# Performance work log

Hardware: AMD Instinct MI355X
Metric: run time of the kernel (lower is better)

Reference implementation:

```python
import jax, jax.numpy as jnp
import numpy as np

N, E, IN, H0, H1 = 50000, 1600000, 64, 64, 128


def _gcn(h, W, b, row, col):
    # PyG GCNConv, add_self_loops=False, unit edge weights:
    # out[col] += d^{-1/2}[row] * d^{-1/2}[col] * (h @ W)[row]; bias added after aggregation
    n = h.shape[0]
    deg = jnp.zeros((n,), h.dtype).at[col].add(jnp.ones((row.shape[0],), h.dtype))
    dinv = jnp.where(deg > 0, jax.lax.rsqrt(jnp.maximum(deg, 1e-12)), 0.0)
    norm = (dinv[row] * dinv[col])[:, None]  # [E,1]
    m = h @ W  # transform before propagate (small GEMM)
    out = jnp.zeros((n, W.shape[1]), h.dtype).at[col].add(norm * m[row])
    return out + b


def _bn(h, g, b):
    # BatchNorm1d training-mode math (biased variance), eps=1e-5
    mu = h.mean(0)
    var = ((h - mu) ** 2).mean(0)
    return g * (h - mu) * jax.lax.rsqrt(var + 1e-5) + b


def _san(h):
    return jnp.nan_to_num(h, nan=0.0, posinf=100.0, neginf=-100.0)


def _slice(x, ei, W0, b0, W1, b1, res1, g0, be0, g1, be1):
    row, col = ei[0], ei[1]
    # layer 0: conv -> bn -> relu -> (dropout=eval identity) -> residual (Identity, 64==64) -> nan_to_num
    h1 = _san(jax.nn.relu(_bn(_gcn(x, W0, b0, row, col), g0, be0)) + x)
    # layer 1 (last): conv -> bn -> residual (Linear proj 64->128, no bias) -> nan_to_num
    h2 = _san(_bn(_gcn(h1, W1, b1, row, col), g1, be1) + h1 @ res1)
    return h2


def setup_inputs() -> dict:
    k = jax.random.split(jax.random.key(0), 16)
    f = lambda kk, sh, s: jax.random.normal(kk, sh, jnp.float32) * s
    return {
        "x": f(k[0], (N, IN), 1.0),
        "edge_index0": jax.random.randint(k[1], (2, E), 0, N),
        "edge_index1": jax.random.randint(k[2], (2, E), 0, N),
        "w0_s0": f(k[3], (IN, H0), 0.1), "b0_s0": jnp.zeros((H0,), jnp.float32),
        "w1_s0": f(k[4], (H0, H1), 0.1), "b1_s0": jnp.zeros((H1,), jnp.float32),
        "res1_s0": f(k[5], (H0, H1), 0.1),
        "w0_s1": f(k[6], (IN, H0), 0.1), "b0_s1": jnp.zeros((H0,), jnp.float32),
        "w1_s1": f(k[7], (H0, H1), 0.1), "b1_s1": jnp.zeros((H1,), jnp.float32),
        "res1_s1": f(k[8], (H0, H1), 0.1),
        "bn_g0": jnp.ones((H0,), jnp.float32), "bn_b0": jnp.zeros((H0,), jnp.float32),
        "bn_g1": jnp.ones((H1,), jnp.float32), "bn_b1": jnp.zeros((H1,), jnp.float32),
        "fc1_w": f(k[9], (2 * H1, H1), 0.1), "fc1_b": jnp.zeros((H1,), jnp.float32),
        "fc2_w": f(k[10], (H1, 2), 0.1), "fc2_b": jnp.zeros((2,), jnp.float32),
    }


def reference(x, edge_index0, edge_index1,
              w0_s0, b0_s0, w1_s0, b1_s0, res1_s0,
              w0_s1, b0_s1, w1_s1, b1_s1, res1_s1,
              bn_g0, bn_b0, bn_g1, bn_b1,
              fc1_w, fc1_b, fc2_w, fc2_b):
    out0 = _slice(x, edge_index0, w0_s0, b0_s0, w1_s0, b1_s0, res1_s0, bn_g0, bn_b0, bn_g1, bn_b1)
    out1 = _slice(x, edge_index1, w0_s1, b0_s1, w1_s1, b1_s1, res1_s1, bn_g0, bn_b0, bn_g1, bn_b1)
    combined = jnp.concatenate([out0, out1], axis=1)  # [N, 2*H1]
    h = jax.nn.relu(combined @ fc1_w + fc1_b)  # dropout is eval-mode identity
    logits = h @ fc2_w + fc2_b
    return logits, jax.nn.softmax(logits, axis=1)
```

## Files before the change

kernel.cpp:

```cpp
#include <hip/hip_runtime.h>
#include <hip/hip_bf16.h>
#include <math.h>


typedef short v8s __attribute__((ext_vector_type(8)));
typedef float f32x4 __attribute__((ext_vector_type(4)));

#define BSTRIDE 10240

__device__ __forceinline__ float sanf(float v) {
    if (v != v) return 0.f;
    if (isinf(v)) return v > 0.f ? 100.f : -100.f;
    return v;
}

__device__ __forceinline__ unsigned short bf16of(float v) {
    __hip_bfloat16 h = __float2bfloat16(v);
    return *(unsigned short*)&h;
}
__device__ __forceinline__ unsigned pack2(float lo, float hi) {
    return (unsigned)bf16of(lo) | ((unsigned)bf16of(hi) << 16);
}
__device__ __forceinline__ float uflo(unsigned u) { return __uint_as_float(u << 16); }
__device__ __forceinline__ float ufhi(unsigned u) { return __uint_as_float(u & 0xFFFF0000u); }

__device__ __forceinline__ void packone(const float* __restrict__ src, unsigned* __restrict__ dst,
                                        int L, int Khalf, int F) {
    int c = L / Khalf, kp = L - c * Khalf;
    dst[L] = pack2(src[(2 * kp) * F + c], src[(2 * kp + 1) * F + c]);
}

__global__ __launch_bounds__(256) void prep_kernel(const float* __restrict__ w0_0,
                                                   const float* __restrict__ w0_1,
                                                   const float* __restrict__ w1_0,
                                                   const float* __restrict__ w1_1,
                                                   const float* __restrict__ r_0,
                                                   const float* __restrict__ r_1,
                                                   const float* __restrict__ fc1,
                                                   unsigned* __restrict__ wpk,
                                                   int* __restrict__ bcnt,
                                                   float* __restrict__ sums) {
    int gid = blockIdx.x * 256 + threadIdx.x;
    if (gid < 512) bcnt[gid] = 0;
    if (gid < 8192) sums[gid] = 0.f;
    if (gid < 2048)       packone(w0_0, wpk + 0,     gid - 0,     32, 64);
    else if (gid < 4096)  packone(w0_1, wpk + 2048,  gid - 2048,  32, 64);
    else if (gid < 8192)  packone(w1_0, wpk + 4096,  gid - 4096,  32, 128);
    else if (gid < 12288) packone(w1_1, wpk + 8192,  gid - 8192,  32, 128);
    else if (gid < 16384) packone(r_0,  wpk + 12288, gid - 12288, 32, 128);
    else if (gid < 20480) packone(r_1,  wpk + 16384, gid - 16384, 32, 128);
    else if (gid < 36864) packone(fc1,  wpk + 20480, gid - 20480, 128, 128);
}


__global__ __launch_bounds__(512) void kC_bin(const int* __restrict__ ei0,
                                              const int* __restrict__ ei1,
                                              int* __restrict__ bcnt,
                                              unsigned* __restrict__ binned,
                                              int E, int n) {
    __shared__ int cnt[512];
    __shared__ int base[512];
    int t = threadIdx.x;
    cnt[t] = 0;
    int E2 = 2 * E;
    int e0 = blockIdx.x * 8192;
    unsigned pk[16];
    int bk[16];
    __syncthreads();
#pragma unroll
    for (int j = 0; j < 16; ++j) {
        int ge = e0 + t + j * 512;
        bk[j] = -1;
        if (ge < E2) {
            int slice = ge >= E;
            const int* ei = slice ? ei1 : ei0;
            int e = ge - slice * E;
            int col = ei[E + e], row = ei[e];
            int gcol = slice * n + col;
            bk[j] = gcol >> 8;
            pk[j] = (unsigned)row | (((unsigned)gcol & 255u) << 16);
            atomicAdd(&cnt[bk[j]], 1);
        }
    }
    __syncthreads();
    {
        int c = cnt[t];
        base[t] = c ? atomicAdd(&bcnt[t], c) : 0;
    }
    __syncthreads();
    cnt[t] = 0;
    __syncthreads();
#pragma unroll
    for (int j = 0; j < 16; ++j) {
        if (bk[j] >= 0) {
            int loc = atomicAdd(&cnt[bk[j]], 1);
            int off = base[bk[j]] + loc;
            if (off < BSTRIDE) binned[(size_t)bk[j] * BSTRIDE + off] = pk[j];
        }
    }
}

__global__ __launch_bounds__(512) void kD_build(const unsigned* __restrict__ binned,
                                                const int* __restrict__ bcnt,
                                                const float* __restrict__ x,
                                                int* __restrict__ rowptr,
                                                float* __restrict__ dinv,
                                                unsigned short* __restrict__ csr,
                                                unsigned short* __restrict__ xsb,
                                                int n2, int NB) {
    __shared__ int pref[512];
    __shared__ int cnt[256];
    __shared__ int scn[256];
    __shared__ int cur[256];
    __shared__ float ds[256];
    int b = blockIdx.x, t = threadIdx.x;
    int n = n2 >> 1, n64 = n * 64;
    pref[t] = (t < NB) ? bcnt[t] : 0;
    __syncthreads();
    for (int off = 1; off < 512; off <<= 1) {
        int u = (t >= off) ? pref[t - off] : 0;
        __syncthreads();
        pref[t] += u;
        __syncthreads();
    }
    int s = (b > 0) ? pref[b - 1] : 0;
    int e = pref[b];
    int m = e - s;
    const unsigned* seg = binned + (size_t)b * BSTRIDE;
    if (t < 256) cnt[t] = 0;
    __syncthreads();
    for (int i = t; i < m; i += 512) atomicAdd(&cnt[(seg[i] >> 16) & 255], 1);
    __syncthreads();
    int v = (t < 256) ? cnt[t] : 0;
    if (t < 256) scn[t] = v;
    __syncthreads();
    for (int off = 1; off < 256; off <<= 1) {
        int u = (t < 256 && t >= off) ? scn[t - off] : 0;
        __syncthreads();
        if (t < 256) scn[t] += u;
        __syncthreads();
    }
    if (t < 256) {
        int excl = scn[t] - v;
        int gcol = b * 256 + t;
        float dv = v > 0 ? rsqrtf((float)v) : 0.f;
        ds[t] = dv;
        if (gcol < n2) {
            rowptr[gcol] = s + excl;
            dinv[gcol] = dv;
        }
        cur[t] = excl;
    }
    __syncthreads();
    for (int i = t; i < m; i += 512) {
        unsigned p = seg[i];
        int cl = (p >> 16) & 255;
        int pos = s + atomicAdd(&cur[cl], 1);
        csr[pos] = (unsigned short)(p & 0xFFFFu);
    }
    if (b == NB - 1 && t == 0) rowptr[n2] = e;
    for (int k = t; k < 2048; k += 512) {
        int gl = k >> 3, segk = k & 7;
        int gcol = b * 256 + gl;
        if (gcol >= n2) continue;
        float d = ds[gl];
        int slice = gcol >= n;
        int row = gcol - slice * n;
        const float* xp = x + (size_t)row * 64 + segk * 8;
        float4 v0 = *(const float4*)xp;
        float4 v1 = *(const float4*)(xp + 4);
        uint4 o;
        o.x = pack2(v0.x * d, v0.y * d); o.y = pack2(v0.z * d, v0.w * d);
        o.z = pack2(v1.x * d, v1.y * d); o.w = pack2(v1.z * d, v1.w * d);
        *(uint4*)&xsb[(size_t)slice * n64 + (size_t)row * 64 + segk * 8] = o;
    }
}


#define LOAD8(U, IDX)                                                       \
    do {                                                                    \
        _Pragma("unroll") for (int j = 0; j < 8; ++j) {                     \
            int r = __shfl((IDX), j, 8);                                    \
            (U)[j] = *(const uint4*)&mb[(size_t)r * 64 + l * 8];            \
        }                                                                   \
    } while (0)
#define ZPAD8(U, BB)                                                        \
    do {                                                                    \
        _Pragma("unroll") for (int j = 0; j < 8; ++j)                       \
            if ((BB) + j >= e) { (U)[j].x = 0; (U)[j].y = 0;                \
                                 (U)[j].z = 0; (U)[j].w = 0; }              \
    } while (0)
#define ACC8(U)                                                             \
    do {                                                                    \
        _Pragma("unroll") for (int j = 0; j < 8; ++j) {                     \
            a0 += uflo((U)[j].x); a1 += ufhi((U)[j].x);                     \
            a2 += uflo((U)[j].y); a3 += ufhi((U)[j].y);                     \
            a4 += uflo((U)[j].z); a5 += ufhi((U)[j].z);                     \
            a6 += uflo((U)[j].w); a7 += ufhi((U)[j].w);                     \
        }                                                                   \
    } while (0)

__global__ __launch_bounds__(256) void gatherbf_kernel(const int* __restrict__ rowptr,
                                                       const unsigned short* __restrict__ csr,
                                                       const unsigned short* __restrict__ xsb,
                                                       const float* __restrict__ dinv,
                                                       unsigned short* __restrict__ outb,
                                                       int n) {
    int blk = blockIdx.x;
    int xcd = blk & 7;
    int slice = (xcd >= 4) ? 1 : 0;
    int rank = (blk >> 3) * 4 + (xcd & 3);
    int nodeLocal = rank * 32 + (threadIdx.x >> 3);
    if (nodeLocal >= n) return;
    int node = slice * n + nodeLocal;
    int l = threadIdx.x & 7;
    const unsigned short* mb = xsb + (size_t)slice * n * 64;
    int s = rowptr[node], e = rowptr[node + 1];
    float a0 = 0.f, a1 = 0.f, a2 = 0.f, a3 = 0.f, a4 = 0.f, a5 = 0.f, a6 = 0.f, a7 = 0.f;
    uint4 uA[8], uB[8];
    int b = s;
    if (b + 8 <= e) {
        int ia = csr[b + l];
        LOAD8(uA, ia);
        int bB = b + 8;
        int ib = (bB + l < e) ? (int)csr[bB + l] : 0;
        while (true) {
            bool hasB = (bB < e);
            if (hasB) {
                LOAD8(uB, ib);
                if (bB + 8 > e) ZPAD8(uB, bB);
            }
            int bA2 = bB + 8;
            if (bA2 < e) ia = (bA2 + l < e) ? (int)csr[bA2 + l] : 0;
            ACC8(uA);
            if (!hasB) break;
            bool hasA2 = (bA2 < e);
            if (hasA2) {
                LOAD8(uA, ia);
                if (bA2 + 8 > e) ZPAD8(uA, bA2);
            }
            int bB2 = bA2 + 8;
            if (bB2 < e) ib = (bB2 + l < e) ? (int)csr[bB2 + l] : 0;
            ACC8(uB);
            if (!hasA2) break;
            bB = bB2;
        }
    } else if (b < e) {
        int ia = (b + l < e) ? (int)csr[b + l] : 0;
        LOAD8(uA, ia);
        ZPAD8(uA, b);
        ACC8(uA);
    }
    float d = dinv[node];
    uint4 o;
    o.x = pack2(a0 * d, a1 * d);
    o.y = pack2(a2 * d, a3 * d);
    o.z = pack2(a4 * d, a5 * d);
    o.w = pack2(a6 * d, a7 * d);
    *(uint4*)&outb[(size_t)node * 64 + l * 8] = o;
}


template <int F>
__global__ __launch_bounds__(256) void mfma_gemmb(const unsigned short* __restrict__ Ab,
                                                  const unsigned* __restrict__ WT0,
                                                  const unsigned* __restrict__ WT1,
                                                  unsigned short* __restrict__ Cb,
                                                  float* __restrict__ sums_base,
                                                  int roff, int n) {
    constexpr int NC = F / 16;
    __shared__ float ls[2 * F];
    __shared__ unsigned short stb[64 * F];
    int BPS = (n + 63) >> 6;
    int slice = blockIdx.x >= BPS;
    int sb = blockIdx.x - slice * BPS;
    const unsigned* WT = slice ? WT1 : WT0;
    int row0 = slice * n + sb * 64;
    int rows = min(64, n - sb * 64);
    for (int i = threadIdx.x; i < 2 * F; i += 256) ls[i] = 0.f;
    int w = threadIdx.x >> 6, lane = threadIdx.x & 63, q = lane >> 4, ln = lane & 15;
    const unsigned* A32 = (const unsigned*)Ab;
    size_t arow = (size_t)(row0 + 16 * w + ln) * 32;
    v8s af0 = *(const v8s*)&A32[arow + q * 4];
    v8s af1 = *(const v8s*)&A32[arow + 16 + q * 4];
    f32x4 acc[NC];
#pragma unroll
    for (int ct = 0; ct < NC; ++ct) acc[ct] = {0.f, 0.f, 0.f, 0.f};
#pragma unroll
    for (int ct = 0; ct < NC; ++ct) {
        v8s b0 = *(const v8s*)&WT[(ct * 16 + ln) * 32 + q * 4];
        v8s b1 = *(const v8s*)&WT[(ct * 16 + ln) * 32 + 16 + q * 4];
        acc[ct] = __builtin_amdgcn_mfma_f32_16x16x32_bf16(af0, b0, acc[ct], 0, 0, 0);
        acc[ct] = __builtin_amdgcn_mfma_f32_16x16x32_bf16(af1, b1, acc[ct], 0, 0, 0);
    }
    __syncthreads();
#pragma unroll
    for (int ct = 0; ct < NC; ++ct) {
        float s1 = 0.f, s2 = 0.f;
        int cc = ct * 16 + ln;
#pragma unroll
        for (int i = 0; i < 4; ++i) {
            int r = 16 * w + q * 4 + i;
            stb[r * F + (cc ^ ((r & 7) << 3))] = bf16of(acc[ct][i]);
            if (r < rows) {
                float v = acc[ct][i];
                s1 += v;
                s2 += v * v;
            }
        }
        s1 += __shfl_xor(s1, 16); s1 += __shfl_xor(s1, 32);
        s2 += __shfl_xor(s2, 16); s2 += __shfl_xor(s2, 32);
        if (q == 0) {
            atomicAdd(&ls[cc], s1);
            atomicAdd(&ls[F + cc], s2);
        }
    }
    __syncthreads();
    {
        constexpr int CPT = F / 4;
        int rr = threadIdx.x >> 2, sg = threadIdx.x & 3;
        if (rr < rows) {
            int swz = (rr & 7) << 3;
            int cb = sg * CPT;
            uint4* dst = (uint4*)(Cb + (size_t)(row0 + rr) * F + cb);
#pragma unroll
            for (int jj = 0; jj < CPT / 8; ++jj)
                dst[jj] = *(const uint4*)&stb[rr * F + ((cb + jj * 8) ^ swz)];
        }
    }
    if (threadIdx.x < F) {
        float* dst = sums_base + (blockIdx.x & 7) * 1024 + roff + slice * 2 * F;
        unsafeAtomicAdd(&dst[threadIdx.x], ls[threadIdx.x]);
        unsafeAtomicAdd(&dst[F + threadIdx.x], ls[F + threadIdx.x]);
    }
}

__global__ __launch_bounds__(256) void apply0_kernel(const unsigned short* __restrict__ t0b,
                                                     const float* __restrict__ x,
                                                     const float* __restrict__ sums_base,
                                                     const float* __restrict__ g,
                                                     const float* __restrict__ be,
                                                     const float* __restrict__ dinv,
                                                     unsigned short* __restrict__ h1b,
                                                     unsigned short* __restrict__ h1sb,
                                                     int n64, int total, int n) {
    __shared__ float sc[256];
    int t = threadIdx.x;
    if (t < 128) {
        int slice = t >> 6, f = t & 63;
        float s1 = 0.f, s2 = 0.f;
#pragma unroll
        for (int r = 0; r < 8; ++r) {
            const float* src = sums_base + r * 1024 + 512 + slice * 128;
            s1 += src[f];
            s2 += src[64 + f];
        }
        float inv_n = 1.0f / (float)n;
        float mu = s1 * inv_n;
        float var = fmaxf(s2 * inv_n - mu * mu, 0.f);
        float scale = g[f] * rsqrtf(var + 1e-5f);
        sc[slice * 128 + f] = scale;
        sc[slice * 128 + 64 + f] = be[f] - mu * scale;
    }
    __syncthreads();
    int i8 = (blockIdx.x * 256 + t) * 8;
    if (i8 >= total) return;
    int slice = i8 >= n64;
    int f0 = i8 & 63;
    const float* scp = sc + slice * 128;
    uint4 tv = *(const uint4*)&t0b[i8];
    const float* xp = x + (i8 - slice * n64);
    float4 x0 = *(const float4*)xp;
    float4 x1 = *(const float4*)(xp + 4);
    float4 s0 = *(const float4*)&scp[f0];
    float4 s1 = *(const float4*)&scp[f0 + 4];
    float4 g0 = *(const float4*)&scp[64 + f0];
    float4 g1 = *(const float4*)&scp[64 + f0 + 4];
    float d = dinv[i8 >> 6];
    float tvv[8] = {uflo(tv.x), ufhi(tv.x), uflo(tv.y), ufhi(tv.y),
                    uflo(tv.z), ufhi(tv.z), uflo(tv.w), ufhi(tv.w)};
    float sa[8] = {s0.x, s0.y, s0.z, s0.w, s1.x, s1.y, s1.z, s1.w};
    float sh[8] = {g0.x, g0.y, g0.z, g0.w, g1.x, g1.y, g1.z, g1.w};
    float xv[8] = {x0.x, x0.y, x0.z, x0.w, x1.x, x1.y, x1.z, x1.w};
    unsigned po[4], ps[4];
#pragma unroll
    for (int j = 0; j < 4; ++j) {
        float a = sanf(fmaxf(fmaf(tvv[2 * j], sa[2 * j], sh[2 * j]), 0.f) + xv[2 * j]);
        float b = sanf(fmaxf(fmaf(tvv[2 * j + 1], sa[2 * j + 1], sh[2 * j + 1]), 0.f) + xv[2 * j + 1]);
        po[j] = pack2(a, b);
        ps[j] = pack2(a * d, b * d);
    }
    *(uint4*)&h1b[i8] = *(uint4*)po;
    *(uint4*)&h1sb[i8] = *(uint4*)ps;
}

__global__ __launch_bounds__(256) void apply1_head(const unsigned short* __restrict__ h1b,
                                                   const unsigned short* __restrict__ Tb,
                                                   const unsigned* __restrict__ RT0,
                                                   const unsigned* __restrict__ RT1,
                                                   const unsigned* __restrict__ FT,
                                                   const float* __restrict__ sums_base,
                                                   const float* __restrict__ g,
                                                   const float* __restrict__ be,
                                                   const float* __restrict__ fc1_b,
                                                   const float* __restrict__ w2,
                                                   const float* __restrict__ b2,
                                                   float* __restrict__ out, int n) {
    __shared__ float st[64 * 128];
    __shared__ unsigned short cmb[64 * 256];
    __shared__ float scl[512];
    int t = threadIdx.x;
    int row0l = blockIdx.x * 64;
    int rows = min(64, n - row0l);
    {
        int slice = t >> 7, f = t & 127;
        float s1 = 0.f, s2 = 0.f;
#pragma unroll
        for (int r = 0; r < 8; ++r) {
            const float* src = sums_base + r * 1024 + slice * 256;
            s1 += src[f];
            s2 += src[128 + f];
        }
        float inv_n = 1.0f / (float)n;
        float mu = s1 * inv_n;
        float var = fmaxf(s2 * inv_n - mu * mu, 0.f);
        float scale = g[f] * rsqrtf(var + 1e-5f);
        scl[slice * 256 + f] = scale;
        scl[slice * 256 + 128 + f] = be[f] - mu * scale;
    }
    int w = t >> 6, lane = t & 63, q = lane >> 4, ln = lane & 15;
#pragma unroll
    for (int slice = 0; slice < 2; ++slice) {
        const unsigned* WT = slice ? RT1 : RT0;
        int row0 = slice * n + row0l;
        const unsigned* A32 = (const unsigned*)h1b;
        size_t arow = (size_t)(row0 + 16 * w + ln) * 32;
        v8s af0 = *(const v8s*)&A32[arow + q * 4];
        v8s af1 = *(const v8s*)&A32[arow + 16 + q * 4];
        f32x4 acc[8];
#pragma unroll
        for (int ct = 0; ct < 8; ++ct) acc[ct] = {0.f, 0.f, 0.f, 0.f};
#pragma unroll
        for (int ct = 0; ct < 8; ++ct) {
            v8s b0 = *(const v8s*)&WT[(ct * 16 + ln) * 32 + q * 4];
            v8s b1 = *(const v8s*)&WT[(ct * 16 + ln) * 32 + 16 + q * 4];
            acc[ct] = __builtin_amdgcn_mfma_f32_16x16x32_bf16(af0, b0, acc[ct], 0, 0, 0);
            acc[ct] = __builtin_amdgcn_mfma_f32_16x16x32_bf16(af1, b1, acc[ct], 0, 0, 0);
        }
#pragma unroll
        for (int ct = 0; ct < 8; ++ct) {
            int cc = ct * 16 + ln;
#pragma unroll
            for (int i = 0; i < 4; ++i) {
                int r = 16 * w + q * 4 + i;
                st[r * 128 + (cc ^ ((r & 7) << 2))] = acc[ct][i];
            }
        }
        __syncthreads();
        int rr = t >> 2, sg = t & 3;
        if (rr < rows) {
            int swz = (rr & 7) << 2;
            int swzB = (rr & 7) << 4;
            int rg = row0 + rr;
            const uint4* tbp = (const uint4*)(Tb + (size_t)rg * 128 + sg * 32);
            const float* scb = scl + slice * 256 + sg * 32;
            char* cp = (char*)(cmb + rr * 256);
#pragma unroll
            for (int jj = 0; jj < 4; ++jj) {
                uint4 tv = tbp[jj];
                int base = sg * 32 + jj * 8;
                float4 a0 = *(const float4*)&st[rr * 128 + (base ^ swz)];
                float4 a1 = *(const float4*)&st[rr * 128 + ((base + 4) ^ swz)];
                float4 s0 = *(const float4*)&scb[jj * 8];
                float4 s1 = *(const float4*)&scb[jj * 8 + 4];
                float4 h0 = *(const float4*)&scb[128 + jj * 8];
                float4 h1v = *(const float4*)&scb[128 + jj * 8 + 4];
                float o0 = sanf(fmaf(uflo(tv.x), s0.x, h0.x) + a0.x);
                float o1 = sanf(fmaf(ufhi(tv.x), s0.y, h0.y) + a0.y);
                float o2 = sanf(fmaf(uflo(tv.y), s0.z, h0.z) + a0.z);
                float o3 = sanf(fmaf(ufhi(tv.y), s0.w, h0.w) + a0.w);
                float o4 = sanf(fmaf(uflo(tv.z), s1.x, h1v.x) + a1.x);
                float o5 = sanf(fmaf(ufhi(tv.z), s1.y, h1v.y) + a1.y);
                float o6 = sanf(fmaf(uflo(tv.w), s1.z, h1v.z) + a1.z);
                float o7 = sanf(fmaf(ufhi(tv.w), s1.w, h1v.w) + a1.w);
                uint4 ov;
                ov.x = pack2(o0, o1);
                ov.y = pack2(o2, o3);
                ov.z = pack2(o4, o5);
                ov.w = pack2(o6, o7);
                *(uint4*)(cp + ((slice * 256 + sg * 64 + jj * 16) ^ swzB)) = ov;
            }
        }
        __syncthreads();
    }
    {
        int rowLocal = 16 * w + ln;
        const char* cr = (const char*)(cmb + rowLocal * 256);
        int swzR = (rowLocal & 7) << 4;
        f32x4 acc[8];
#pragma unroll
        for (int ct = 0; ct < 8; ++ct) acc[ct] = {0.f, 0.f, 0.f, 0.f};
#pragma unroll
        for (int kt = 0; kt < 4; ++kt) {
            v8s af0 = *(const v8s*)(cr + ((kt * 128 + q * 16) ^ swzR));
            v8s af1 = *(const v8s*)(cr + ((kt * 128 + 64 + q * 16) ^ swzR));
#pragma unroll
            for (int ct = 0; ct < 8; ++ct) {
                v8s b0 = *(const v8s*)&FT[(ct * 16 + ln) * 128 + kt * 32 + q * 4];
                v8s b1 = *(const v8s*)&FT[(ct * 16 + ln) * 128 + kt * 32 + 16 + q * 4];
                acc[ct] = __builtin_amdgcn_mfma_f32_16x16x32_bf16(af0, b0, acc[ct], 0, 0, 0);
                acc[ct] = __builtin_amdgcn_mfma_f32_16x16x32_bf16(af1, b1, acc[ct], 0, 0, 0);
            }
        }
        float p0[4] = {0.f, 0.f, 0.f, 0.f}, p1[4] = {0.f, 0.f, 0.f, 0.f};
#pragma unroll
        for (int ct = 0; ct < 8; ++ct) {
            int c = ct * 16 + ln;
            float bi = fc1_b[c];
            float w20 = w2[c * 2], w21 = w2[c * 2 + 1];
#pragma unroll
            for (int i = 0; i < 4; ++i) {
                float h = fmaxf(acc[ct][i] + bi, 0.f);
                p0[i] = fmaf(h, w20, p0[i]);
                p1[i] = fmaf(h, w21, p1[i]);
            }
        }
#pragma unroll
        for (int i = 0; i < 4; ++i) {
#pragma unroll
            for (int msk = 1; msk < 16; msk <<= 1) {
                p0[i] += __shfl_xor(p0[i], msk);
                p1[i] += __shfl_xor(p1[i], msk);
            }
        }
        if (ln == 0) {
            float bb0 = b2[0], bb1 = b2[1];
#pragma unroll
            for (int i = 0; i < 4; ++i) {
                int r = 16 * w + q * 4 + i;
                if (r >= rows) continue;
                int R = row0l + r;
                float l0 = p0[i] + bb0, l1 = p1[i] + bb1;
                float mx = fmaxf(l0, l1);
                float e0 = expf(l0 - mx), e1 = expf(l1 - mx);
                float inv = 1.0f / (e0 + e1);
                out[(size_t)R * 2] = l0;
                out[(size_t)R * 2 + 1] = l1;
                out[(size_t)2 * n + R * 2] = e0 * inv;
                out[(size_t)2 * n + R * 2 + 1] = e1 * inv;
            }
        }
    }
}

static inline int cdiv(int a, int b) { return (a + b - 1) / b; }

extern "C" void kernel_launch(void* const* d_in, const int* in_sizes, int n_in,
                              void* d_out, int out_size, void* d_ws, size_t ws_size,
                              hipStream_t stream) {
    const float* x       = (const float*)d_in[0];
    const int*   ei0     = (const int*)d_in[1];
    const int*   ei1     = (const int*)d_in[2];
    const float* w0_s0   = (const float*)d_in[3];
    const float* w1_s0   = (const float*)d_in[5];
    const float* res1_s0 = (const float*)d_in[7];
    const float* w0_s1   = (const float*)d_in[8];
    const float* w1_s1   = (const float*)d_in[10];
    const float* res1_s1 = (const float*)d_in[12];
    const float* bn_g0   = (const float*)d_in[13];
    const float* bn_b0   = (const float*)d_in[14];
    const float* bn_g1   = (const float*)d_in[15];
    const float* bn_b1   = (const float*)d_in[16];
    const float* fc1_w   = (const float*)d_in[17];
    const float* fc1_b   = (const float*)d_in[18];
    const float* fc2_w   = (const float*)d_in[19];
    const float* fc2_b   = (const float*)d_in[20];
    float* out = (float*)d_out;

    int n = in_sizes[0] / 64;
    int E = in_sizes[1] / 2;
    int n2 = 2 * n, E2 = 2 * E;
    int n64 = n * 64;
    int NB = cdiv(n2, 256);
    int BPS = cdiv(n, 64);
    int GB = 8 * cdiv(cdiv(n, 32), 4);

    float* X1 = (float*)d_ws;
    float* S  = X1 + (size_t)n2 * 64;
    unsigned short* Gb   = (unsigned short*)(S + (size_t)n2 * 64);
    unsigned short* h1b  = Gb + (size_t)n2 * 64;
    unsigned short* comb = h1b + (size_t)n2 * 64;
    unsigned short* xsb  = comb + (size_t)n * 256;
    float* dinv = (float*)(xsb + (size_t)n * 128);
    float* sums = dinv + n2;
    float* scsh = sums + 8192;
    unsigned* wpk = (unsigned*)(scsh + 512);
    unsigned short* csr = (unsigned short*)(wpk + 36864);
    int* rowptr = (int*)(csr + (size_t)E2);
    int* bcnt   = rowptr + (n2 + 1);
    unsigned short* t0b = (unsigned short*)X1;
    unsigned short* Tb  = (unsigned short*)X1;
    unsigned* binned = (unsigned*)comb;
    unsigned short* h1sb = (unsigned short*)S;
    unsigned* w0T0 = wpk + 0,    *w0T1 = wpk + 2048;
    unsigned* w1T0 = wpk + 4096, *w1T1 = wpk + 8192;
    unsigned* rT0  = wpk + 12288,*rT1  = wpk + 16384;
    unsigned* fT   = wpk + 20480;

    prep_kernel<<<144, 256, 0, stream>>>(w0_s0, w0_s1, w1_s0, w1_s1,
                                         res1_s0, res1_s1, fc1_w, wpk, bcnt, sums);
    kC_bin<<<cdiv(E2, 8192), 512, 0, stream>>>(ei0, ei1, bcnt, binned, E, n);
    kD_build<<<NB, 512, 0, stream>>>(binned, bcnt, x, rowptr, dinv, csr, xsb, n2, NB);

    gatherbf_kernel<<<GB, 256, 0, stream>>>(rowptr, csr, xsb, dinv, Gb, n);
    mfma_gemmb<64><<<2 * BPS, 256, 0, stream>>>(Gb, w0T0, w0T1, t0b, sums, 512, n);
    apply0_kernel<<<cdiv(2 * n64, 2048), 256, 0, stream>>>(t0b, x, sums, bn_g0, bn_b0,
                                                           dinv, h1b, h1sb, n64, 2 * n64, n);

    gatherbf_kernel<<<GB, 256, 0, stream>>>(rowptr, csr, h1sb, dinv, Gb, n);
    mfma_gemmb<128><<<2 * BPS, 256, 0, stream>>>(Gb, w1T0, w1T1, Tb, sums, 0, n);

    apply1_head<<<BPS, 256, 0, stream>>>(h1b, Tb, rT0, rT1, fT, sums, bn_g1, bn_b1,
                                         fc1_b, fc2_w, fc2_b, out, n);
}
```

Baseline: 347.2 us.

## Store layer-1 GEMM output in MFMA fragment layout and fuse residual in registers

The 128-wide GEMM for layer 1 now writes its accumulators straight out in MFMA fragment order instead of staging them through shared memory into row-major bf16. The head kernel reads that fragment layout, so each lane's BN-scaled T values line up with its own residual-GEMM accumulators. This drops the 32KB float staging buffer and two block barriers in the head. The trade-off is smaller, less coalesced 8-byte writes and reads and a layout tied to a 64-row block.

```diff
diff --git a/kernel.cpp b/kernel.cpp
--- a/kernel.cpp
+++ b/kernel.cpp
@@ -260,14 +260,13 @@
     *(uint4*)&outb[(size_t)node * 64 + l * 8] = o;
 }
 
-
-template <int F>
-__global__ __launch_bounds__(256) void mfma_gemmb(const unsigned short* __restrict__ Ab,
-                                                  const unsigned* __restrict__ WT0,
-                                                  const unsigned* __restrict__ WT1,
-                                                  unsigned short* __restrict__ Cb,
-                                                  float* __restrict__ sums_base,
-                                                  int roff, int n) {
+__global__ __launch_bounds__(256) void mfma_gemmb64(const unsigned short* __restrict__ Ab,
+                                                    const unsigned* __restrict__ WT0,
+                                                    const unsigned* __restrict__ WT1,
+                                                    unsigned short* __restrict__ Cb,
+                                                    float* __restrict__ sums_base,
+                                                    int roff, int n) {
+    constexpr int F = 64;
     constexpr int NC = F / 16;
     __shared__ float ls[2 * F];
     __shared__ unsigned short stb[64 * F];
@@ -332,6 +331,69 @@
         float* dst = sums_base + (blockIdx.x & 7) * 1024 + roff + slice * 2 * F;
         unsafeAtomicAdd(&dst[threadIdx.x], ls[threadIdx.x]);
         unsafeAtomicAdd(&dst[F + threadIdx.x], ls[F + threadIdx.x]);
+    }
+}
+
+__global__ __launch_bounds__(256) void mfma_gemmb128f(const unsigned short* __restrict__ Ab,
+                                                      const unsigned* __restrict__ WT0,
+                                                      const unsigned* __restrict__ WT1,
+                                                      unsigned short* __restrict__ Tfrag,
+                                                      float* __restrict__ sums_base,
+                                                      int n) {
+    __shared__ float ls[256];
+    int BPS = (n + 63) >> 6;
+    int slice = blockIdx.x >= BPS;
+    int sb = blockIdx.x - slice * BPS;
+    const unsigned* WT = slice ? WT1 : WT0;
+    int row0 = slice * n + sb * 64;
+    int rows = min(64, n - sb * 64);
+    for (int i = threadIdx.x; i < 256; i += 256) ls[i] = 0.f;
+    int w = threadIdx.x >> 6, lane = threadIdx.x & 63, q = lane >> 4, ln = lane & 15;
+    const unsigned* A32 = (const unsigned*)Ab;
+    size_t arow = (size_t)(row0 + 16 * w + ln) * 32;
+    v8s af0 = *(const v8s*)&A32[arow + q * 4];
+    v8s af1 = *(const v8s*)&A32[arow + 16 + q * 4];
+    f32x4 acc[8];
+#pragma unroll
+    for (int ct = 0; ct < 8; ++ct) acc[ct] = {0.f, 0.f, 0.f, 0.f};
+#pragma unroll
+    for (int ct = 0; ct < 8; ++ct) {
+        v8s b0 = *(const v8s*)&WT[(ct * 16 + ln) * 32 + q * 4];
+        v8s b1 = *(const v8s*)&WT[(ct * 16 + ln) * 32 + 16 + q * 4];
+        acc[ct] = __builtin_amdgcn_mfma_f32_16x16x32_bf16(af0, b0, acc[ct], 0, 0, 0);
+        acc[ct] = __builtin_amdgcn_mfma_f32_16x16x32_bf16(af1, b1, acc[ct], 0, 0, 0);
+    }
+    __syncthreads();
+    unsigned short* tb = Tfrag + (size_t)blockIdx.x * 8192;
+#pragma unroll
+    for (int ct = 0; ct < 8; ++ct) {
+        uint2 o2;
+        o2.x = pack2(acc[ct][0], acc[ct][1]);
+        o2.y = pack2(acc[ct][2], acc[ct][3]);
+        *(uint2*)&tb[((ct * 4 + w) * 64 + lane) * 4] = o2;
+        float s1 = 0.f, s2 = 0.f;
+        int cc = ct * 16 + ln;
+#pragma unroll
+        for (int i = 0; i < 4; ++i) {
+            int r = 16 * w + q * 4 + i;
+            if (r < rows) {
+                float v = acc[ct][i];
+                s1 += v;
+                s2 += v * v;
+            }
+        }
+        s1 += __shfl_xor(s1, 16); s1 += __shfl_xor(s1, 32);
+        s2 += __shfl_xor(s2, 16); s2 += __shfl_xor(s2, 32);
+        if (q == 0) {
+            atomicAdd(&ls[cc], s1);
+            atomicAdd(&ls[128 + cc], s2);
+        }
+    }
+    __syncthreads();
+    if (threadIdx.x < 128) {
+        float* dst = sums_base + (blockIdx.x & 7) * 1024 + slice * 256;
+        unsafeAtomicAdd(&dst[threadIdx.x], ls[threadIdx.x]);
+        unsafeAtomicAdd(&dst[128 + threadIdx.x], ls[128 + threadIdx.x]);
     }
 }
 
@@ -395,7 +457,7 @@
 }
 
 __global__ __launch_bounds__(256) void apply1_head(const unsigned short* __restrict__ h1b,
-                                                   const unsigned short* __restrict__ Tb,
+                                                   const unsigned short* __restrict__ Tfrag,
                                                    const unsigned* __restrict__ RT0,
                                                    const unsigned* __restrict__ RT1,
                                                    const unsigned* __restrict__ FT,
@@ -406,10 +468,10 @@
                                                    const float* __restrict__ w2,
                                                    const float* __restrict__ b2,
                                                    float* __restrict__ out, int n) {
-    __shared__ float st[64 * 128];
     __shared__ unsigned short cmb[64 * 256];
     __shared__ float scl[512];
     int t = threadIdx.x;
+    int BPS = (n + 63) >> 6;
     int row0l = blockIdx.x * 64;
     int rows = min(64, n - row0l);
     {
@@ -428,7 +490,9 @@
         scl[slice * 256 + f] = scale;
         scl[slice * 256 + 128 + f] = be[f] - mu * scale;
     }
+    __syncthreads();
     int w = t >> 6, lane = t & 63, q = lane >> 4, ln = lane & 15;
+    int rbase = 16 * w + q * 4;
 #pragma unroll
     for (int slice = 0; slice < 2; ++slice) {
         const unsigned* WT = slice ? RT1 : RT0;
@@ -447,63 +511,36 @@
             acc[ct] = __builtin_amdgcn_mfma_f32_16x16x32_bf16(af0, b0, acc[ct], 0, 0, 0);
             acc[ct] = __builtin_amdgcn_mfma_f32_16x16x32_bf16(af1, b1, acc[ct], 0, 0, 0);
         }
+        const unsigned short* tb = Tfrag + (size_t)(slice * BPS + blockIdx.x) * 8192;
+        const float* scb = scl + slice * 256;
 #pragma unroll
         for (int ct = 0; ct < 8; ++ct) {
-            int cc = ct * 16 + ln;
-#pragma unroll
-            for (int i = 0; i < 4; ++i) {
-                int r = 16 * w + q * 4 + i;
-                st[r * 128 + (cc ^ ((r & 7) << 2))] = acc[ct][i];
-            }
-        }
-        __syncthreads();
-        int rr = t >> 2, sg = t & 3;
-        if (rr < rows) {
-            int swz = (rr & 7) << 2;
-            int swzB = (rr & 7) << 4;
-            int rg = row0 + rr;
-            const uint4* tbp = (const uint4*)(Tb + (size_t)rg * 128 + sg * 32);
-            const float* scb = scl + slice * 256 + sg * 32;
-            char* cp = (char*)(cmb + rr * 256);
-#pragma unroll
-            for (int jj = 0; jj < 4; ++jj) {
-                uint4 tv = tbp[jj];
-                int base = sg * 32 + jj * 8;
-                float4 a0 = *(const float4*)&st[rr * 128 + (base ^ swz)];
-                float4 a1 = *(const float4*)&st[rr * 128 + ((base + 4) ^ swz)];
-                float4 s0 = *(const float4*)&scb[jj * 8];
-                float4 s1 = *(const float4*)&scb[jj * 8 + 4];
-                float4 h0 = *(const float4*)&scb[128 + jj * 8];
-                float4 h1v = *(const float4*)&scb[128 + jj * 8 + 4];
-                float o0 = sanf(fmaf(uflo(tv.x), s0.x, h0.x) + a0.x);
-                float o1 = sanf(fmaf(ufhi(tv.x), s0.y, h0.y) + a0.y);
-                float o2 = sanf(fmaf(uflo(tv.y), s0.z, h0.z) + a0.z);
-                float o3 = sanf(fmaf(ufhi(tv.y), s0.w, h0.w) + a0.w);
-                float o4 = sanf(fmaf(uflo(tv.z), s1.x, h1v.x) + a1.x);
-                float o5 = sanf(fmaf(ufhi(tv.z), s1.y, h1v.y) + a1.y);
-                float o6 = sanf(fmaf(uflo(tv.w), s1.z, h1v.z) + a1.z);
-                float o7 = sanf(fmaf(ufhi(tv.w), s1.w, h1v.w) + a1.w);
-                uint4 ov;
-                ov.x = pack2(o0, o1);
-                ov.y = pack2(o2, o3);
-                ov.z = pack2(o4, o5);
-                ov.w = pack2(o6, o7);
-                *(uint4*)(cp + ((slice * 256 + sg * 64 + jj * 16) ^ swzB)) = ov;
-            }
-        }
-        __syncthreads();
-    }
+            uint2 tf = *(const uint2*)&tb[((ct * 4 + w) * 64 + lane) * 4];
+            int c = ct * 16 + ln;
+            float sc_ = scb[c], sh_ = scb[128 + c];
+            float o0 = sanf(fmaf(uflo(tf.x), sc_, sh_) + acc[ct][0]);
+            float o1 = sanf(fmaf(ufhi(tf.x), sc_, sh_) + acc[ct][1]);
+            float o2 = sanf(fmaf(uflo(tf.y), sc_, sh_) + acc[ct][2]);
+            float o3 = sanf(fmaf(ufhi(tf.y), sc_, sh_) + acc[ct][3]);
+            int gc = slice * 128 + c;
+            cmb[(rbase + 0) * 256 + (gc ^ (((rbase + 0) & 7) << 3))] = bf16of(o0);
+            cmb[(rbase + 1) * 256 + (gc ^ (((rbase + 1) & 7) << 3))] = bf16of(o1);
+            cmb[(rbase + 2) * 256 + (gc ^ (((rbase + 2) & 7) << 3))] = bf16of(o2);
+            cmb[(rbase + 3) * 256 + (gc ^ (((rbase + 3) & 7) << 3))] = bf16of(o3);
+        }
+    }
+    __syncthreads();
     {
         int rowLocal = 16 * w + ln;
-        const char* cr = (const char*)(cmb + rowLocal * 256);
-        int swzR = (rowLocal & 7) << 4;
+        const unsigned short* cr = cmb + rowLocal * 256;
+        int swzR = (rowLocal & 7) << 3;
         f32x4 acc[8];
 #pragma unroll
         for (int ct = 0; ct < 8; ++ct) acc[ct] = {0.f, 0.f, 0.f, 0.f};
 #pragma unroll
         for (int kt = 0; kt < 4; ++kt) {
-            v8s af0 = *(const v8s*)(cr + ((kt * 128 + q * 16) ^ swzR));
-            v8s af1 = *(const v8s*)(cr + ((kt * 128 + 64 + q * 16) ^ swzR));
+            v8s af0 = *(const v8s*)&cr[(kt * 64 + q * 8) ^ swzR];
+            v8s af1 = *(const v8s*)&cr[(kt * 64 + 32 + q * 8) ^ swzR];
 #pragma unroll
             for (int ct = 0; ct < 8; ++ct) {
                 v8s b0 = *(const v8s*)&FT[(ct * 16 + ln) * 128 + kt * 32 + q * 4];
@@ -586,7 +623,7 @@
     int GB = 8 * cdiv(cdiv(n, 32), 4);
 
     float* X1 = (float*)d_ws;
-    float* S  = X1 + (size_t)n2 * 64;
+    float* S  = X1 + (size_t)2 * BPS * 4096;
     unsigned short* Gb   = (unsigned short*)(S + (size_t)n2 * 64);
     unsigned short* h1b  = Gb + (size_t)n2 * 64;
     unsigned short* comb = h1b + (size_t)n2 * 64;
@@ -599,7 +636,7 @@
     int* rowptr = (int*)(csr + (size_t)E2);
     int* bcnt   = rowptr + (n2 + 1);
     unsigned short* t0b = (unsigned short*)X1;
-    unsigned short* Tb  = (unsigned short*)X1;
+    unsigned short* Tfrag = (unsigned short*)X1;
     unsigned* binned = (unsigned*)comb;
     unsigned short* h1sb = (unsigned short*)S;
     unsigned* w0T0 = wpk + 0,    *w0T1 = wpk + 2048;
@@ -613,13 +650,13 @@
     kD_build<<<NB, 512, 0, stream>>>(binned, bcnt, x, rowptr, dinv, csr, xsb, n2, NB);
 
     gatherbf_kernel<<<GB, 256, 0, stream>>>(rowptr, csr, xsb, dinv, Gb, n);
-    mfma_gemmb<64><<<2 * BPS, 256, 0, stream>>>(Gb, w0T0, w0T1, t0b, sums, 512, n);
+    mfma_gemmb64<<<2 * BPS, 256, 0, stream>>>(Gb, w0T0, w0T1, t0b, sums, 512, n);
     apply0_kernel<<<cdiv(2 * n64, 2048), 256, 0, stream>>>(t0b, x, sums, bn_g0, bn_b0,
                                                            dinv, h1b, h1sb, n64, 2 * n64, n);
 
     gatherbf_kernel<<<GB, 256, 0, stream>>>(rowptr, csr, h1sb, dinv, Gb, n);
-    mfma_gemmb<128><<<2 * BPS, 256, 0, stream>>>(Gb, w1T0, w1T1, Tb, sums, 0, n);
-
-    apply1_head<<<BPS, 256, 0, stream>>>(h1b, Tb, rT0, rT1, fT, sums, bn_g1, bn_b1,
+    mfma_gemmb128f<<<2 * BPS, 256, 0, stream>>>(Gb, w1T0, w1T1, Tfrag, sums, n);
+
+    apply1_head<<<BPS, 256, 0, stream>>>(h1b, Tfrag, rT0, rT1, fT, sums, bn_g1, bn_b1,
                                          fc1_b, fc2_w, fc2_b, out, n);
 }
```

After: 342.8 us. About the same (-1.3%).
